# Performance work log

Measured on AMD Instinct MI355X. Metric: run time of the kernel, lower is better.

The kernel has to match this reference:

```python
import jax, jax.numpy as jnp
import numpy as np

H = 1024        # hidden_size
NH = 16         # num_heads
HD = H // NH    # head_dim
NS = 3          # num_strata


def setup_inputs() -> dict:
    key = jax.random.key(0)
    ks = jax.random.split(key, 12)
    s = 1.0 / np.sqrt(H)
    inp = {
        "hidden_states": jax.random.normal(ks[0], (2, 2048, H), dtype=jnp.float32),
        "Wq": jax.random.uniform(ks[1], (H, H), minval=-s, maxval=s, dtype=jnp.float32),
        "bq": jax.random.uniform(ks[2], (H,), minval=-s, maxval=s, dtype=jnp.float32),
        "Wk": jax.random.uniform(ks[3], (H, H), minval=-s, maxval=s, dtype=jnp.float32),
        "bk": jax.random.uniform(ks[4], (H,), minval=-s, maxval=s, dtype=jnp.float32),
        "Wv": jax.random.uniform(ks[5], (H, H), minval=-s, maxval=s, dtype=jnp.float32),
        "bv": jax.random.uniform(ks[6], (H,), minval=-s, maxval=s, dtype=jnp.float32),
        "Ws": jax.random.uniform(ks[7], (NS, H, H), minval=-s, maxval=s, dtype=jnp.float32),
        "bs": jax.random.uniform(ks[8], (NS, H), minval=-s, maxval=s, dtype=jnp.float32),
        "Wo": jax.random.uniform(ks[9], (H, H), minval=-s, maxval=s, dtype=jnp.float32),
        "bo": jax.random.uniform(ks[10], (H,), minval=-s, maxval=s, dtype=jnp.float32),
    }
    return inp


def reference(hidden_states, Wq, bq, Wk, bk, Wv, bv, Ws, bs, Wo, bo):
    B, S, _ = hidden_states.shape
    # torch nn.Linear: y = x @ W.T + b
    q = hidden_states @ Wq.T + bq
    k = hidden_states @ Wk.T + bk
    v = hidden_states @ Wv.T + bv
    # [B, NH, S, HD]
    q = q.reshape(B, S, NH, HD).transpose(0, 2, 1, 3)
    k = k.reshape(B, S, NH, HD).transpose(0, 2, 1, 3)
    v = v.reshape(B, S, NH, HD).transpose(0, 2, 1, 3)
    scores = jnp.einsum('bhqd,bhkd->bhqk', q, k) / jnp.sqrt(jnp.float32(HD))
    attn = jax.nn.softmax(scores, axis=-1)
    out = jnp.einsum('bhqk,bhkd->bhqd', attn, v)
    attn_output = out.transpose(0, 2, 1, 3).reshape(B, S, H)
    # stratum projections, averaged: [NS, B, S, H] -> mean over strata
    strata = jnp.einsum('bsh,ngh->nbsg', attn_output, Ws) + bs[:, None, None, :]
    enhanced = strata.mean(axis=0)
    output = enhanced @ Wo.T + bo
    return output
```

## Files before the change

### kernel.cpp

```cpp
#include <hip/hip_runtime.h>
#include <stdint.h>

typedef __attribute__((ext_vector_type(8))) short short8;
typedef __attribute__((ext_vector_type(4))) short short4v;
typedef __attribute__((ext_vector_type(4))) float f32x4;
typedef __attribute__((ext_vector_type(2))) unsigned int u32x2;
typedef unsigned int u32;
typedef const __attribute__((address_space(1))) u32* gas_ptr;
typedef __attribute__((address_space(3))) u32* las_ptr;

#define QSCALE 0.18033688011112042f

__device__ inline short f2bf(float x) {
    u32 u = __float_as_uint(x);
    u = u + 0x7FFFu + ((u >> 16) & 1u);
    return (short)(u >> 16);
}
__device__ inline void gload16(const void* g, const void* l) {
    __builtin_amdgcn_global_load_lds((gas_ptr)g, (las_ptr)l, 16, 0, 0);
}

__global__ __launch_bounds__(256) void prep(const float* __restrict__ X,
                                            const float* __restrict__ Wq,
                                            const float* __restrict__ Wk,
                                            const float* __restrict__ Wv,
                                            const float* __restrict__ Wo,
                                            const float* __restrict__ Ws,
                                            const float* __restrict__ bs,
                                            const float* __restrict__ bo,
                                            short* __restrict__ Xb,
                                            short* __restrict__ Wcat,
                                            short* __restrict__ Wob,
                                            short* __restrict__ WmT,
                                            float* __restrict__ bc) {
    __shared__ short T[64][65];
    const int tid = threadIdx.x;
    const int bid = blockIdx.x;
    if (bid < 8192) {
        const float* src;
        short* dst;
        int rel;
        if (bid < 4096)      { src = X;  dst = Xb;                rel = bid; }
        else if (bid < 5120) { src = Wq; dst = Wcat;              rel = bid - 4096; }
        else if (bid < 6144) { src = Wk; dst = Wcat + (1 << 20);  rel = bid - 5120; }
        else if (bid < 7168) { src = Wv; dst = Wcat + (2 << 20);  rel = bid - 6144; }
        else                 { src = Wo; dst = Wob;               rel = bid - 7168; }
        int i = (rel * 256 + tid) * 4;
        float4 v = *(const float4*)&src[i];
        short4v o;
        o[0] = f2bf(v.x); o[1] = f2bf(v.y); o[2] = f2bf(v.z); o[3] = f2bf(v.w);
        *(short4v*)&dst[i] = o;
    } else if (bid < 8448) {
        const int id = bid - 8192;
        const int gx = (id & 15) * 64, jy = (id >> 4) * 64;
        const int HH = 1 << 20;
        for (int e = tid; e < 4096; e += 256) {
            int j = e >> 6, g = e & 63;
            int idx = (jy + j) * 1024 + gx + g;
            float v = (Ws[idx] + Ws[idx + HH] + Ws[idx + 2 * HH]) * (1.0f / 3.0f);
            T[g][j] = f2bf(v);
        }
        __syncthreads();
        for (int e = tid; e < 4096; e += 256) {
            int g = e >> 6, j = e & 63;
            WmT[(long)(gx + g) * 1024 + jy + j] = T[g][j];
        }
    } else {
        const int lane = tid & 63;
        const int n = (bid - 8448) * 4 + (tid >> 6);
        float acc = 0.0f;
        for (int j0 = 0; j0 < 1024; j0 += 64) {
            int j = j0 + lane;
            float bm = (bs[j] + bs[j + 1024] + bs[j + 2048]) * (1.0f / 3.0f);
            acc += Wo[(long)n * 1024 + j] * bm;
        }
#pragma unroll
        for (int off = 1; off < 64; off <<= 1) acc += __shfl_xor(acc, off, 64);
        if (lane == 0) bc[n] = acc + bo[n];
    }
}

__global__ __launch_bounds__(256) void gemm_qkvwc(const short* __restrict__ Xb,
                                                  const short* __restrict__ Wcat,
                                                  const short* __restrict__ Wob,
                                                  const short* __restrict__ WmT,
                                                  const float* __restrict__ bq,
                                                  const float* __restrict__ bk,
                                                  const float* __restrict__ bv,
                                                  short* __restrict__ Qb,
                                                  short* __restrict__ Kb,
                                                  short* __restrict__ Vt,
                                                  short* __restrict__ Wc) {
    __shared__ short As[64 * 64];
    __shared__ short Bs[128 * 64];
    const int K = 1024;
    const int tid  = threadIdx.x;
    const int lane = tid & 63;
    const int wave = tid >> 6;
    const int quad = lane >> 4;
    const int l16  = lane & 15;
    const int bid = blockIdx.x;
    const short *A, *W;
    int m0, n0, sel;
    if (bid < 1536) {
        sel = bid >> 9;
        int r = bid & 511;
        m0 = (r >> 3) * 64;
        n0 = (r & 7) * 128;
        A = Xb;
        W = Wcat + (long)sel * (1 << 20);
    } else {
        int w = bid - 1536;
        sel = 3;
        m0 = (w >> 3) * 64;
        n0 = (w & 7) * 128;
        A = Wob;
        W = WmT;
    }
    const int wm = (wave >> 1) * 32;
    const int wn = (wave & 1) * 64;

    f32x4 acc[2][4] = {};
    const int sr = tid >> 3;
    const int scol = (((tid & 7) ^ (sr & 7)) << 3);
    const int fo_a = ((quad ^ (l16 & 7)) << 3);
    const int fo_b = (((4 + quad) ^ (l16 & 7)) << 3);

    for (int k0 = 0; k0 < K; k0 += 64) {
#pragma unroll
        for (int i = 0; i < 2; i++) {
            int r = i * 32 + sr;
            gload16(&A[(long)(m0 + r) * K + k0 + scol], &As[i * 2048 + wave * 512]);
        }
#pragma unroll
        for (int i = 0; i < 4; i++) {
            int r = i * 32 + sr;
            gload16(&W[(long)(n0 + r) * K + k0 + scol], &Bs[i * 2048 + wave * 512]);
        }
        __syncthreads();
        short8 bfr[4][2];
#pragma unroll
        for (int ni = 0; ni < 4; ni++) {
            const int row = wn + ni * 16 + l16;
            bfr[ni][0] = *(short8*)&Bs[row * 64 + fo_a];
            bfr[ni][1] = *(short8*)&Bs[row * 64 + fo_b];
        }
#pragma unroll
        for (int mi = 0; mi < 2; mi++) {
            const int row = wm + mi * 16 + l16;
            short8 af0 = *(short8*)&As[row * 64 + fo_a];
            short8 af1 = *(short8*)&As[row * 64 + fo_b];
#pragma unroll
            for (int ni = 0; ni < 4; ni++) {
                acc[mi][ni] = __builtin_amdgcn_mfma_f32_16x16x32_bf16(af0, bfr[ni][0],
                                                                      acc[mi][ni], 0, 0, 0);
                acc[mi][ni] = __builtin_amdgcn_mfma_f32_16x16x32_bf16(af1, bfr[ni][1],
                                                                      acc[mi][ni], 0, 0, 0);
            }
        }
        __syncthreads();
    }

#pragma unroll
    for (int mi = 0; mi < 2; mi++) {
#pragma unroll
        for (int ni = 0; ni < 4; ni++) {
            const int n = n0 + wn + ni * 16 + l16;
            const int mbase = m0 + wm + mi * 16 + quad * 4;
            float bv2 = 0.0f;
            if (sel == 0) bv2 = bq[n];
            else if (sel == 1) bv2 = bk[n];
            else if (sel == 2) bv2 = bv[n];
            if (sel == 2) {
                short4v pk;
#pragma unroll
                for (int r = 0; r < 4; r++) pk[r] = f2bf(acc[mi][ni][r] + bv2);
                long addr = ((long)(mbase >> 11) << 21) + (long)n * 2048 + (mbase & 2047);
                *(short4v*)&Vt[addr] = pk;
            } else if (sel == 0) {
#pragma unroll
                for (int r = 0; r < 4; r++)
                    Qb[(long)(mbase + r) * 1024 + n] = f2bf((acc[mi][ni][r] + bv2) * QSCALE);
            } else {
                short* C = (sel == 1) ? Kb : Wc;
#pragma unroll
                for (int r = 0; r < 4; r++)
                    C[(long)(mbase + r) * 1024 + n] = f2bf(acc[mi][ni][r] + bv2);
            }
        }
    }
}

__global__ __launch_bounds__(256) void attn_kernel(const short* __restrict__ Q,
                                                   const short* __restrict__ Kb,
                                                   const short* __restrict__ Vt,
                                                   short* __restrict__ O) {
    __shared__ short Ks[2][64 * 64];
    __shared__ short Vs[64 * 64];
    __shared__ short Ps[64 * 64];
    const int tid  = threadIdx.x;
    const int lane = tid & 63;
    const int w    = tid >> 6;
    const int quad = lane >> 4;
    const int l16  = lane & 15;
    const int sw   = l16 & 7;
    const int q0 = blockIdx.x * 64;
    const int h  = blockIdx.y;
    const int b  = blockIdx.z;

    short8 qB[4][2];
#pragma unroll
    for (int ni = 0; ni < 4; ni++) {
        const long base = (long)(b * 2048 + q0 + ni * 16 + l16) * 1024 + h * 64 + quad * 8;
        qB[ni][0] = *(const short8*)&Q[base];
        qB[ni][1] = *(const short8*)&Q[base + 32];
    }

    const int sr = tid >> 3;
    const int scol = (((tid & 7) ^ (sr & 7)) << 3);
    const short* Kp = Kb + (long)(b * 2048) * 1024 + h * 64;
    const short* Vp = Vt + ((long)b << 21) + (long)h * 64 * 2048;

    const int arow = w * 16 + l16;
    const int ao0 = ((quad ^ sw) << 3);
    const int ao1 = (((4 + quad) ^ sw) << 3);
    const int pchunk = ((w * 2 + (quad >> 1)) ^ sw) << 3;
    const int psub = (quad & 1) << 2;

    f32x4 o[4] = {};
    float lsum[4] = {0.0f, 0.0f, 0.0f, 0.0f};

#pragma unroll
    for (int i = 0; i < 2; i++) {
        int r = i * 32 + sr;
        gload16(&Kp[(long)r * 1024 + scol], &Ks[0][i * 2048 + w * 512]);
    }
    __syncthreads();

    for (int kt = 0; kt < 32; kt++) {
        const int cur = kt & 1;
        const int kb = kt * 64;

#pragma unroll
        for (int i = 0; i < 2; i++) {
            int r = i * 32 + sr;
            gload16(&Vp[(long)r * 2048 + kb + scol], &Vs[i * 2048 + w * 512]);
        }

        short8 ak0 = *(short8*)&Ks[cur][arow * 64 + ao0];
        short8 ak1 = *(short8*)&Ks[cur][arow * 64 + ao1];
#pragma unroll
        for (int ni = 0; ni < 4; ni++) {
            f32x4 s = {};
            s = __builtin_amdgcn_mfma_f32_16x16x32_bf16(ak0, qB[ni][0], s, 0, 0, 0);
            s = __builtin_amdgcn_mfma_f32_16x16x32_bf16(ak1, qB[ni][1], s, 0, 0, 0);
            float p0 = __builtin_amdgcn_exp2f(s[0]);
            float p1 = __builtin_amdgcn_exp2f(s[1]);
            float p2 = __builtin_amdgcn_exp2f(s[2]);
            float p3 = __builtin_amdgcn_exp2f(s[3]);
            lsum[ni] += (p0 + p1) + (p2 + p3);
            u32 a0 = __float_as_uint(p0) + 0x8000u;
            u32 a1 = __float_as_uint(p1) + 0x8000u;
            u32 a2 = __float_as_uint(p2) + 0x8000u;
            u32 a3 = __float_as_uint(p3) + 0x8000u;
            u32x2 wv;
            wv[0] = __builtin_amdgcn_perm(a1, a0, 0x07060302u);
            wv[1] = __builtin_amdgcn_perm(a3, a2, 0x07060302u);
            *(u32x2*)&Ps[(ni * 16 + l16) * 64 + pchunk + psub] = wv;
        }

        __syncthreads();

        if (kt < 31) {
            const int kbn = kb + 64;
#pragma unroll
            for (int i = 0; i < 2; i++) {
                int r = i * 32 + sr;
                gload16(&Kp[(long)(kbn + r) * 1024 + scol],
                        &Ks[cur ^ 1][i * 2048 + w * 512]);
            }
        }

        short8 av0 = *(short8*)&Vs[arow * 64 + ao0];
        short8 av1 = *(short8*)&Vs[arow * 64 + ao1];
#pragma unroll
        for (int ni = 0; ni < 4; ni++) {
            short8 pb0 = *(short8*)&Ps[(ni * 16 + l16) * 64 + ao0];
            short8 pb1 = *(short8*)&Ps[(ni * 16 + l16) * 64 + ao1];
            o[ni] = __builtin_amdgcn_mfma_f32_16x16x32_bf16(av0, pb0, o[ni], 0, 0, 0);
            o[ni] = __builtin_amdgcn_mfma_f32_16x16x32_bf16(av1, pb1, o[ni], 0, 0, 0);
        }

        __syncthreads();
    }

    float* Lred = (float*)Ps;
#pragma unroll
    for (int ni = 0; ni < 4; ni++) {
        lsum[ni] += __shfl_xor(lsum[ni], 16, 64);
        lsum[ni] += __shfl_xor(lsum[ni], 32, 64);
    }
    if (lane < 16) {
#pragma unroll
        for (int ni = 0; ni < 4; ni++) Lred[w * 64 + ni * 16 + l16] = lsum[ni];
    }
    __syncthreads();
#pragma unroll
    for (int ni = 0; ni < 4; ni++) {
        const int qi = ni * 16 + l16;
        const float tot = ((Lred[qi] + Lred[64 + qi]) + (Lred[128 + qi] + Lred[192 + qi]));
        const float inv = 1.0f / tot;
        const long token = b * 2048 + q0 + ni * 16 + l16;
        short4v pk;
#pragma unroll
        for (int r = 0; r < 4; r++) pk[r] = f2bf(o[ni][r] * inv);
        *(short4v*)&O[token * 1024 + h * 64 + w * 16 + quad * 4] = pk;
    }
}

__global__ __launch_bounds__(256) void gemm_final(const short* __restrict__ A,
                                                  const short* __restrict__ W,
                                                  const float* __restrict__ bias,
                                                  float* __restrict__ C) {
    __shared__ short As[64 * 64];
    __shared__ short Bs[128 * 64];
    const int K = 1024;
    const int tid  = threadIdx.x;
    const int lane = tid & 63;
    const int wave = tid >> 6;
    const int quad = lane >> 4;
    const int l16  = lane & 15;
    const int bid = blockIdx.x;
    const int m0 = (bid >> 3) * 64;
    const int n0 = (bid & 7) * 128;
    const int wm = (wave >> 1) * 32;
    const int wn = (wave & 1) * 64;

    f32x4 acc[2][4] = {};
    const int sr = tid >> 3;
    const int scol = (((tid & 7) ^ (sr & 7)) << 3);
    const int fo_a = ((quad ^ (l16 & 7)) << 3);
    const int fo_b = (((4 + quad) ^ (l16 & 7)) << 3);

    for (int k0 = 0; k0 < K; k0 += 64) {
#pragma unroll
        for (int i = 0; i < 2; i++) {
            int r = i * 32 + sr;
            gload16(&A[(long)(m0 + r) * K + k0 + scol], &As[i * 2048 + wave * 512]);
        }
#pragma unroll
        for (int i = 0; i < 4; i++) {
            int r = i * 32 + sr;
            gload16(&W[(long)(n0 + r) * K + k0 + scol], &Bs[i * 2048 + wave * 512]);
        }
        __syncthreads();
        short8 bfr[4][2];
#pragma unroll
        for (int ni = 0; ni < 4; ni++) {
            const int row = wn + ni * 16 + l16;
            bfr[ni][0] = *(short8*)&Bs[row * 64 + fo_a];
            bfr[ni][1] = *(short8*)&Bs[row * 64 + fo_b];
        }
#pragma unroll
        for (int mi = 0; mi < 2; mi++) {
            const int row = wm + mi * 16 + l16;
            short8 af0 = *(short8*)&As[row * 64 + fo_a];
            short8 af1 = *(short8*)&As[row * 64 + fo_b];
#pragma unroll
            for (int ni = 0; ni < 4; ni++) {
                acc[mi][ni] = __builtin_amdgcn_mfma_f32_16x16x32_bf16(af0, bfr[ni][0],
                                                                      acc[mi][ni], 0, 0, 0);
                acc[mi][ni] = __builtin_amdgcn_mfma_f32_16x16x32_bf16(af1, bfr[ni][1],
                                                                      acc[mi][ni], 0, 0, 0);
            }
        }
        __syncthreads();
    }

#pragma unroll
    for (int mi = 0; mi < 2; mi++) {
#pragma unroll
        for (int ni = 0; ni < 4; ni++) {
            const int n = n0 + wn + ni * 16 + l16;
            const float bv = bias[n];
            const int mbase = m0 + wm + mi * 16 + quad * 4;
#pragma unroll
            for (int r = 0; r < 4; r++)
                C[(long)(mbase + r) * 1024 + n] = acc[mi][ni][r] + bv;
        }
    }
}

extern "C" void kernel_launch(void* const* d_in, const int* in_sizes, int n_in,
                              void* d_out, int out_size, void* d_ws, size_t ws_size,
                              hipStream_t stream) {
    const float* X  = (const float*)d_in[0];
    const float* Wq = (const float*)d_in[1];
    const float* bq = (const float*)d_in[2];
    const float* Wk = (const float*)d_in[3];
    const float* bk = (const float*)d_in[4];
    const float* Wv = (const float*)d_in[5];
    const float* bv = (const float*)d_in[6];
    const float* Ws = (const float*)d_in[7];
    const float* bs = (const float*)d_in[8];
    const float* Wo = (const float*)d_in[9];
    const float* bo = (const float*)d_in[10];

    char* ws = (char*)d_ws;
    const long MB = 1 << 20;
    short* Xb   = (short*)(ws + 0 * MB);
    short* Wcat = (short*)(ws + 8 * MB);
    short* WmT  = (short*)(ws + 14 * MB);
    short* Wob  = (short*)(ws + 16 * MB);
    short* Wc   = (short*)(ws + 18 * MB);
    float* bc   = (float*)(ws + 20 * MB);
    short* Qb   = (short*)(ws + 21 * MB);
    short* Kbf  = (short*)(ws + 29 * MB);
    short* Vtb  = (short*)(ws + 37 * MB);
    short* AO   = Xb;

    dim3 bb(256);

    prep<<<dim3(8704), bb, 0, stream>>>(X, Wq, Wk, Wv, Wo, Ws, bs, bo,
                                        Xb, Wcat, Wob, WmT, bc);
    gemm_qkvwc<<<dim3(1664), bb, 0, stream>>>(Xb, Wcat, Wob, WmT, bq, bk, bv,
                                              Qb, Kbf, Vtb, Wc);
    attn_kernel<<<dim3(32, 16, 2), bb, 0, stream>>>(Qb, Kbf, Vtb, AO);
    gemm_final<<<dim3(512), bb, 0, stream>>>(AO, Wc, bc, (float*)d_out);
}
```

Measured before the change: 227.6 us.

## Feed P from registers into PV MFMA and split-K reduce across waves

```diff
diff --git a/kernel.cpp b/kernel.cpp
--- a/kernel.cpp
+++ b/kernel.cpp
@@ -10,6 +10,12 @@
 typedef __attribute__((address_space(3))) u32* las_ptr;
 
 #define QSCALE 0.18033688011112042f
+
+#if defined(__HIP_DEVICE_COMPILE__)
+#if !__has_builtin(__builtin_amdgcn_mfma_f32_16x16x16bf16_1k)
+#error "missing 16x16x16 bf16 mfma builtin on device"
+#endif
+#endif
 
 __device__ inline short f2bf(float x) {
     u32 u = __float_as_uint(x);
@@ -191,13 +197,12 @@
     }
 }
 
-__global__ __launch_bounds__(256) void attn_kernel(const short* __restrict__ Q,
-                                                   const short* __restrict__ Kb,
-                                                   const short* __restrict__ Vt,
-                                                   short* __restrict__ O) {
+__global__ __launch_bounds__(256, 4) void attn_kernel(const short* __restrict__ Q,
+                                                      const short* __restrict__ Kb,
+                                                      const short* __restrict__ Vt,
+                                                      short* __restrict__ O) {
     __shared__ short Ks[2][64 * 64];
     __shared__ short Vs[64 * 64];
-    __shared__ short Ps[64 * 64];
     const int tid  = threadIdx.x;
     const int lane = tid & 63;
     const int w    = tid >> 6;
@@ -224,10 +229,9 @@
     const int arow = w * 16 + l16;
     const int ao0 = ((quad ^ sw) << 3);
     const int ao1 = (((4 + quad) ^ sw) << 3);
-    const int pchunk = ((w * 2 + (quad >> 1)) ^ sw) << 3;
-    const int psub = (quad & 1) << 2;
-
-    f32x4 o[4] = {};
+    const int vco = (((w * 2 + (quad >> 1)) ^ sw) << 3) + ((quad & 1) << 2);
+
+    f32x4 o[4][4] = {};
     float lsum[4] = {0.0f, 0.0f, 0.0f, 0.0f};
 
 #pragma unroll
@@ -249,6 +253,7 @@
 
         short8 ak0 = *(short8*)&Ks[cur][arow * 64 + ao0];
         short8 ak1 = *(short8*)&Ks[cur][arow * 64 + ao1];
+        short4v pb[4];
 #pragma unroll
         for (int ni = 0; ni < 4; ni++) {
             f32x4 s = {};
@@ -259,14 +264,12 @@
             float p2 = __builtin_amdgcn_exp2f(s[2]);
             float p3 = __builtin_amdgcn_exp2f(s[3]);
             lsum[ni] += (p0 + p1) + (p2 + p3);
-            u32 a0 = __float_as_uint(p0) + 0x8000u;
-            u32 a1 = __float_as_uint(p1) + 0x8000u;
-            u32 a2 = __float_as_uint(p2) + 0x8000u;
-            u32 a3 = __float_as_uint(p3) + 0x8000u;
-            u32x2 wv;
-            wv[0] = __builtin_amdgcn_perm(a1, a0, 0x07060302u);
-            wv[1] = __builtin_amdgcn_perm(a3, a2, 0x07060302u);
-            *(u32x2*)&Ps[(ni * 16 + l16) * 64 + pchunk + psub] = wv;
+            u32x2 pw;
+            pw[0] = __builtin_amdgcn_perm(__float_as_uint(p1) + 0x8000u,
+                                          __float_as_uint(p0) + 0x8000u, 0x07060302u);
+            pw[1] = __builtin_amdgcn_perm(__float_as_uint(p3) + 0x8000u,
+                                          __float_as_uint(p2) + 0x8000u, 0x07060302u);
+            pb[ni] = *(short4v*)&pw;
         }
 
         __syncthreads();
@@ -281,20 +284,19 @@
             }
         }
 
-        short8 av0 = *(short8*)&Vs[arow * 64 + ao0];
-        short8 av1 = *(short8*)&Vs[arow * 64 + ao1];
-#pragma unroll
-        for (int ni = 0; ni < 4; ni++) {
-            short8 pb0 = *(short8*)&Ps[(ni * 16 + l16) * 64 + ao0];
-            short8 pb1 = *(short8*)&Ps[(ni * 16 + l16) * 64 + ao1];
-            o[ni] = __builtin_amdgcn_mfma_f32_16x16x32_bf16(av0, pb0, o[ni], 0, 0, 0);
-            o[ni] = __builtin_amdgcn_mfma_f32_16x16x32_bf16(av1, pb1, o[ni], 0, 0, 0);
-        }
-
-        __syncthreads();
-    }
-
-    float* Lred = (float*)Ps;
+#pragma unroll
+        for (int dt = 0; dt < 4; dt++) {
+            short4v av = *(short4v*)&Vs[(dt * 16 + l16) * 64 + vco];
+#pragma unroll
+            for (int ni = 0; ni < 4; ni++)
+                o[dt][ni] = __builtin_amdgcn_mfma_f32_16x16x16bf16_1k(av, pb[ni],
+                                                                     o[dt][ni], 0, 0, 0);
+        }
+
+        __syncthreads();
+    }
+
+    float* red = (float*)Ks;
 #pragma unroll
     for (int ni = 0; ni < 4; ni++) {
         lsum[ni] += __shfl_xor(lsum[ni], 16, 64);
@@ -302,19 +304,40 @@
     }
     if (lane < 16) {
 #pragma unroll
-        for (int ni = 0; ni < 4; ni++) Lred[w * 64 + ni * 16 + l16] = lsum[ni];
+        for (int ni = 0; ni < 4; ni++) red[w * 64 + ni * 16 + l16] = lsum[ni];
     }
     __syncthreads();
+    float inv[4];
 #pragma unroll
     for (int ni = 0; ni < 4; ni++) {
         const int qi = ni * 16 + l16;
-        const float tot = ((Lred[qi] + Lred[64 + qi]) + (Lred[128 + qi] + Lred[192 + qi]));
-        const float inv = 1.0f / tot;
-        const long token = b * 2048 + q0 + ni * 16 + l16;
-        short4v pk;
-#pragma unroll
-        for (int r = 0; r < 4; r++) pk[r] = f2bf(o[ni][r] * inv);
-        *(short4v*)&O[token * 1024 + h * 64 + w * 16 + quad * 4] = pk;
+        inv[ni] = 1.0f / ((red[qi] + red[64 + qi]) + (red[128 + qi] + red[192 + qi]));
+    }
+    float* slab = red + 256;
+#pragma unroll
+    for (int dt = 0; dt < 4; dt++) {
+        __syncthreads();
+        if (w > 0) {
+#pragma unroll
+            for (int ni = 0; ni < 4; ni++)
+                *(f32x4*)&slab[(w - 1) * 1024 + ni * 256 + l16 * 16 + quad * 4] = o[dt][ni];
+        }
+        __syncthreads();
+        if (w == 0) {
+#pragma unroll
+            for (int ni = 0; ni < 4; ni++) {
+                const int off = ni * 256 + l16 * 16 + quad * 4;
+                f32x4 sum = o[dt][ni];
+                sum += *(f32x4*)&slab[off];
+                sum += *(f32x4*)&slab[1024 + off];
+                sum += *(f32x4*)&slab[2048 + off];
+                short4v pk;
+#pragma unroll
+                for (int r = 0; r < 4; r++) pk[r] = f2bf(sum[r] * inv[ni]);
+                const long token = b * 2048 + q0 + ni * 16 + l16;
+                *(short4v*)&O[token * 1024 + h * 64 + dt * 16 + quad * 4] = pk;
+            }
+        }
     }
 }
 
```

New measurement: 238.6 us. 1.05x slower.
